# Kernel optimization log

Measured on AMD Instinct MI355X. Metric: run time of the kernel, lower is better.

The kernel has to match this reference:

```python
import jax, jax.numpy as jnp
import numpy as np


def gelu(x):
    # custom GELU classes in such repos typically implement the tanh approximation
    return jax.nn.gelu(x, approximate=True)


def setup_inputs() -> dict:
    key = jax.random.key(0)
    ks = jax.random.split(key, 16)
    B, N1, N2, D, H = 4, 1024, 1024, 256, 4
    prev = jax.random.normal(ks[0], (B, N1, D), dtype=jnp.float32)
    curr = jax.random.normal(ks[1], (B, N2, D), dtype=jnp.float32)
    edges = jax.random.randint(ks[2], (B, N1, N2), 0, 2).astype(jnp.int32)

    def lin(k, fan_in, fan_out):
        kw, kb = jax.random.split(k)
        s = 1.0 / np.sqrt(fan_in)
        W = jax.random.uniform(kw, (fan_in, fan_out), jnp.float32, -s, s)
        b = jax.random.uniform(kb, (fan_out,), jnp.float32, -s, s)
        return W, b

    W_pre, b_pre = lin(ks[3], D, 6)
    W_cur, b_cur = lin(ks[4], D, 6)
    W_fuse, b_fuse = lin(ks[5], 12, 4)
    W_ffn, b_ffn = lin(ks[6], 12, 8)
    W_fcc, b_fcc = lin(ks[7], 8, H)
    W_fcg, b_fcg = lin(ks[8], 8, D)
    return {"prev": prev, "curr": curr, "edges": edges,
            "W_pre": W_pre, "b_pre": b_pre, "W_cur": W_cur, "b_cur": b_cur,
            "W_fuse": W_fuse, "b_fuse": b_fuse, "W_ffn": W_ffn, "b_ffn": b_ffn,
            "W_fcc": W_fcc, "b_fcc": b_fcc, "W_fcg": W_fcg, "b_fcg": b_fcg}


def reference(prev, curr, edges, W_pre, b_pre, W_cur, b_cur,
              W_fuse, b_fuse, W_ffn, b_ffn, W_fcc, b_fcc, W_fcg, b_fcg):
    B, N1, D = prev.shape
    N2 = curr.shape[1]
    H = W_fcc.shape[1]
    Dh = D // H
    mask = edges != 0                                   # [B,N1,N2]

    bt_pre = prev @ W_pre + b_pre                       # [B,N1,6]
    bt_cur = curr @ W_cur + b_cur                       # [B,N2,6]
    pair = jnp.concatenate([
        jnp.broadcast_to(bt_pre[:, :, None, :], (B, N1, N2, 6)),
        jnp.broadcast_to(bt_cur[:, None, :, :], (B, N1, N2, 6))], axis=-1)
    c = gelu(pair) @ W_fuse + b_fuse                    # [B,N1,N2,4]
    c = jnp.where(mask[..., None], c, 0.0)

    e1 = (jnp.sum(edges, axis=1) + 1).astype(c.dtype)   # [B,N2]
    d = jnp.sum(c, axis=1)[:, None] / e1[:, None, :, None]
    d = jnp.broadcast_to(d, c.shape)
    e = jnp.broadcast_to(jnp.max(c, axis=1)[:, None], c.shape)
    fused = gelu(jnp.concatenate([c, d, e], axis=-1)) @ W_ffn + b_ffn  # [B,N1,N2,8]

    att = gelu(fused) @ W_fcc + b_fcc                   # [B,N1,N2,H]
    att = jnp.transpose(att, (0, 2, 1, 3))              # [B,N2,N1,H]
    maskT = jnp.transpose(mask, (0, 2, 1))              # [B,N2,N1]
    logits = jnp.where(maskT[..., None], att, -9e15)
    p = jax.nn.softmax(logits, axis=2)                  # softmax over N1 per head
    p = jnp.where(maskT[..., None], p, 0.0)
    # per-head aggregation: head i uses prev columns [i*Dh, (i+1)*Dh)
    res = jnp.einsum('bmnh,bnhd->bmhd', p, prev.reshape(B, N1, H, Dh)).reshape(B, N2, D)

    fused_m = jnp.where(mask[..., None], fused, 0.0)
    g = jnp.sum(fused_m, axis=1) / e1[..., None]        # [B,N2,8]
    return res + gelu(g) @ W_fcg + b_fcg                # [B,N2,D]
```

## Files before the change

### kernel.cpp

```cpp
#include <hip/hip_runtime.h>


using bf16x8 = __attribute__((ext_vector_type(8))) short;
using f32x4  = __attribute__((ext_vector_type(4))) float;
typedef float v2f __attribute__((ext_vector_type(2)));

__device__ __forceinline__ v2f pk_fma(v2f a, v2f b, v2f c){
    return __builtin_elementwise_fma(a, b, c);
}

__device__ __forceinline__ float gelu_f(float x){
    float x2 = x*x;
    float tt = x * __builtin_fmaf(0.044715f, x2, 1.0f);
    float e  = exp2f(-2.3022082f * tt);
    return x * __builtin_amdgcn_rcpf(1.0f + e);
}

__device__ __forceinline__ v2f gelu2(v2f x){
    v2f x2 = x*x;
    v2f tt = x * pk_fma((v2f){0.044715f,0.044715f}, x2, (v2f){1.0f,1.0f});
    float e0 = exp2f(-2.3022082f * tt[0]);
    float e1 = exp2f(-2.3022082f * tt[1]);
    v2f r = { __builtin_amdgcn_rcpf(1.0f + e0),
              __builtin_amdgcn_rcpf(1.0f + e1) };
    return x * r;
}

__device__ __forceinline__ unsigned short f2bf(float f){
    unsigned int u = __float_as_uint(f);
    u += 0x7FFFu + ((u >> 16) & 1u);
    return (unsigned short)(u >> 16);
}

__global__ __launch_bounds__(256) void k_rowsT(
    const float* __restrict__ prev, const float* __restrict__ curr,
    const float* __restrict__ W_pre, const float* __restrict__ b_pre,
    const float* __restrict__ W_cur, const float* __restrict__ b_cur,
    const float* __restrict__ W_fuse, const float* __restrict__ b_fuse,
    float* __restrict__ u_ws, float* __restrict__ v_ws,
    unsigned short* __restrict__ prevT)
{
    __shared__ float tile[64][65];
    int t = threadIdx.x;
    if (blockIdx.x < 2048){
        int gid  = blockIdx.x * 256 + t;
        int wave = gid >> 6;
        int lane = t & 63;
        bool isPrev = wave < 4096;
        int row = isPrev ? wave : (wave - 4096);
        const float* xrow = (isPrev ? prev : curr) + (size_t)row * 256;
        const float* W  = isPrev ? W_pre : W_cur;
        const float* bv = isPrev ? b_pre : b_cur;

        float4 x4 = *reinterpret_cast<const float4*>(xrow + lane*4);
        const float* Wl = W + lane*24;
        float p[6];
        #pragma unroll
        for (int k=0;k<6;++k)
            p[k] = x4.x*Wl[k] + x4.y*Wl[6+k] + x4.z*Wl[12+k] + x4.w*Wl[18+k];
        #pragma unroll
        for (int off=32; off>=1; off>>=1){
            #pragma unroll
            for (int k=0;k<6;++k) p[k] += __shfl_xor(p[k], off, 64);
        }
        if (lane == 0){
            float g[6];
            #pragma unroll
            for(int k=0;k<6;++k) g[k] = gelu_f(p[k] + bv[k]);
            int rb = isPrev ? 0 : 6;
            float o[4];
            #pragma unroll
            for(int kk=0;kk<4;++kk){
                float a = isPrev ? 0.0f : b_fuse[kk];
                #pragma unroll
                for(int k=0;k<6;++k) a += g[k]*W_fuse[(rb+k)*4+kk];
                o[kk]=a;
            }
            float* dst = (isPrev ? u_ws : v_ws) + (size_t)row*4;
            *reinterpret_cast<float4*>(dst) = make_float4(o[0],o[1],o[2],o[3]);
        }
    } else {
        int pbid = blockIdx.x - 2048;
        int b  = pbid >> 6;
        int it = (pbid >> 2) & 15;
        int dt = pbid & 3;
        int i0 = it*64, d0 = dt*64;
        int col = t & 63, rw = t >> 6;
        #pragma unroll
        for (int r = 0; r < 16; ++r){
            int row = rw + 4*r;
            tile[row][col] = prev[((size_t)b*1024 + i0 + row)*256 + d0 + col];
        }
        __syncthreads();
        #pragma unroll
        for (int r = 0; r < 16; ++r){
            int drow = rw + 4*r;
            prevT[((size_t)b*256 + d0 + drow)*1024 + i0 + col]
                = f2bf(tile[col][drow]);
        }
    }
}

__global__ __launch_bounds__(256) void k_cols(
    const int* __restrict__ edges,
    const float* __restrict__ u_ws, const float* __restrict__ v_ws,
    const float* __restrict__ W_ffn, const float* __restrict__ b_ffn,
    float* __restrict__ Gd_ws, float* __restrict__ cnt_ws)
{
    int b  = blockIdx.x >> 6;
    int j0 = (blockIdx.x & 63) * 16;
    int t  = threadIdx.x;
    int jq = t & 3, sl = t >> 2;
    const int*   eb = edges + (size_t)b*1048576 + j0 + jq*4;
    const float* ub = u_ws + (size_t)b*4096;

    int   cnt[4] = {0,0,0,0};
    float S[4][4] = {{0.f}};
    float M[4][4];
    #pragma unroll
    for (int q=0;q<4;++q)
        #pragma unroll
        for (int k=0;k<4;++k) M[q][k] = -3.4e38f;

    #pragma unroll 4
    for (int ii=0; ii<16; ++ii){
        int i = sl*16 + ii;
        int4   e4 = *reinterpret_cast<const int4*>(eb + (size_t)i*1024);
        float4 u4 = *reinterpret_cast<const float4*>(ub + i*4);
        float uu[4] = {u4.x,u4.y,u4.z,u4.w};
        int   ee[4] = {e4.x,e4.y,e4.z,e4.w};
        #pragma unroll
        for (int q=0;q<4;++q){
            bool mk = ee[q]!=0;
            cnt[q] += mk ? 1 : 0;
            #pragma unroll
            for (int k=0;k<4;++k){
                S[q][k] += mk ? uu[k] : 0.0f;
                M[q][k]  = mk ? fmaxf(M[q][k],uu[k]) : M[q][k];
            }
        }
    }
    __shared__ float rS[64][16][4];
    __shared__ float rM[64][16][4];
    __shared__ int   rC[64][16];
    #pragma unroll
    for (int q=0;q<4;++q){
        int c = jq*4+q;
        #pragma unroll
        for (int k=0;k<4;++k){ rS[sl][c][k]=S[q][k]; rM[sl][c][k]=M[q][k]; }
        rC[sl][c]=cnt[q];
    }
    __syncthreads();
    float aS[4], aM[4]; int aC=0; int c2=0, hf=0;
    if (t < 128){
        c2 = t & 15; hf = t >> 4;
        #pragma unroll
        for(int k=0;k<4;++k){ aS[k]=0.f; aM[k]=-3.4e38f; }
        for (int s2=hf*8; s2<hf*8+8; ++s2){
            aC += rC[s2][c2];
            #pragma unroll
            for(int k=0;k<4;++k){ aS[k]+=rS[s2][c2][k]; aM[k]=fmaxf(aM[k],rM[s2][c2][k]); }
        }
    }
    __syncthreads();
    if (t < 128){
        rC[hf][c2]=aC;
        #pragma unroll
        for(int k=0;k<4;++k){ rS[hf][c2][k]=aS[k]; rM[hf][c2][k]=aM[k]; }
    }
    __syncthreads();
    if (t < 16){
        int cc=0; float Sa[4]={0,0,0,0};
        float Ma[4]={-3.4e38f,-3.4e38f,-3.4e38f,-3.4e38f};
        for (int s2=0;s2<8;++s2){
            cc += rC[s2][t];
            #pragma unroll
            for(int k=0;k<4;++k){ Sa[k]+=rS[s2][t][k]; Ma[k]=fmaxf(Ma[k],rM[s2][t][k]); }
        }
        size_t cj = (size_t)b*1024 + j0 + t;
        float4 v4 = *reinterpret_cast<const float4*>(v_ws + cj*4);
        float vv[4]={v4.x,v4.y,v4.z,v4.w};
        float cf = (float)cc, e1 = cf + 1.0f;
        float gd[4], ge[4];
        #pragma unroll
        for(int k=0;k<4;++k){
            float dk = (Sa[k] + cf*vv[k]) / e1;
            float ek;
            if (cc == 0) ek = 0.0f;
            else { float m1 = Ma[k]+vv[k]; ek = (cc < 1024) ? fmaxf(m1, 0.0f) : m1; }
            gd[k]=gelu_f(dk); ge[k]=gelu_f(ek);
        }
        #pragma unroll
        for(int kk=0;kk<8;++kk){
            float a = b_ffn[kk];
            #pragma unroll
            for(int k=0;k<4;++k)
                a += gd[k]*W_ffn[(4+k)*8+kk] + ge[k]*W_ffn[(8+k)*8+kk];
            Gd_ws[cj*8+kk]=a;
        }
        cnt_ws[cj]=cf;
    }
}

template<int SPLIT>
__global__ __launch_bounds__(256) void k_main(
    const unsigned short* __restrict__ prevT, const int* __restrict__ edges,
    const float* __restrict__ u_ws, const float* __restrict__ v_ws,
    const float* __restrict__ Gd_ws,
    const float* __restrict__ W_ffn, const float* __restrict__ W_fcc,
    const float* __restrict__ b_fcc,
    float* __restrict__ Pws, float* __restrict__ Sws, float* __restrict__ Tws)
{
    const int RPB = 1024/SPLIT;
    int bid = blockIdx.x;
    int sp  = bid & (SPLIT-1);
    int jt  = (bid / SPLIT) & 127;
    int b   = bid / (SPLIT*128);
    int j0  = jt*8;
    int t   = threadIdx.x;
    int lane = t & 63;
    int wv   = t >> 6;
    int jl_w = t & 7, il_w = t >> 3;

    __shared__ unsigned short wA[2][4096];
    __shared__ __align__(16) float sU[2][64][4];
    __shared__ float sV[8][4];
    __shared__ float sGd[8][8];

    if (t < 32) (&sV[0][0])[t]  = v_ws[((size_t)b*1024 + j0)*4 + t];
    if (t < 64) (&sGd[0][0])[t] = Gd_ws[((size_t)b*1024 + j0)*8 + t];
    {
        unsigned int* wz = (unsigned int*)wA;
        #pragma unroll
        for (int z=0; z<16; ++z) wz[t + z*256] = 0u;
    }

    const float LOG2E = 1.4426950408889634f;
    v2f W4p[4][4], Wfcp[8][2], bfcp[2];
    #pragma unroll
    for(int k=0;k<4;++k)
        #pragma unroll
        for(int q=0;q<4;++q)
            W4p[k][q] = (v2f){W_ffn[k*8+2*q], W_ffn[k*8+2*q+1]};
    #pragma unroll
    for(int kk=0;kk<8;++kk)
        #pragma unroll
        for(int p2=0;p2<2;++p2)
            Wfcp[kk][p2] = (v2f){W_fcc[kk*4+2*p2]*LOG2E, W_fcc[kk*4+2*p2+1]*LOG2E};
    #pragma unroll
    for(int p2=0;p2<2;++p2)
        bfcp[p2] = (v2f){b_fcc[2*p2]*LOG2E, b_fcc[2*p2+1]*LOG2E};

    f32x4 accm[4];
    #pragma unroll
    for (int tile=0;tile<4;++tile) accm[tile] = (f32x4){0.f,0.f,0.f,0.f};
    f32x4 accs = (f32x4){0.f,0.f,0.f,0.f};
    bf16x8 onesB;
    #pragma unroll
    for (int e=0;e<8;++e) onesB[e] = (short)0x3F80;
    v2f Tp01 = {0,0}, Tp23 = {0,0};

    const int* ebase = edges + (size_t)b*1048576 + j0;
    const int NCH = RPB/64;
    const int base_i0 = sp*RPB;

    int arow = lane & 15, kgrp = lane >> 4;
    int aoff0 = (((wv*16 + arow)*64 + kgrp*8)*2) ^ ((arow & 7) << 4);
    int aoff1 = aoff0 ^ 64;
    const unsigned short* pTbase = prevT
        + ((size_t)b*256 + wv*64 + arow)*1024 + base_i0 + kgrp*8;

    float su_r = u_ws[((size_t)b*1024 + base_i0)*4 + t];
    (&sU[0][0][0])[t] = su_r;
    int egr0 = ebase[(size_t)(base_i0+il_w   )*1024 + jl_w];
    int egr1 = ebase[(size_t)(base_i0+il_w+32)*1024 + jl_w];
    {
        int i0n = base_i0 + ((1 < NCH) ? 64 : 0);
        su_r = u_ws[((size_t)b*1024 + i0n)*4 + t];
    }
    __syncthreads();

    float4 v4p = *reinterpret_cast<const float4*>(&sV[jl_w][0]);
    float4 gd0 = *reinterpret_cast<const float4*>(&sGd[jl_w][0]);
    float4 gd1 = *reinterpret_cast<const float4*>(&sGd[jl_w][4]);

    for (int cc=0; cc<NCH; ++cc){
        int p = cc & 1;
        char* wAp = reinterpret_cast<char*>(wA) + p*8192;

        int eg_c[2] = {egr0, egr1};
        {
            int i0n = base_i0 + ((cc+1 < NCH) ? (cc+1)*64 : 0);
            egr0 = ebase[(size_t)(i0n+il_w   )*1024 + jl_w];
            egr1 = ebase[(size_t)(i0n+il_w+32)*1024 + jl_w];
        }

        #pragma unroll
        for (int r=0;r<2;++r){
            int il = il_w + 32*r;
            int eg = eg_c[r];
            float4 u4 = *reinterpret_cast<const float4*>(&sU[p][il][0]);
            v2f g01 = gelu2((v2f){u4.x + v4p.x, u4.y + v4p.y});
            v2f g23 = gelu2((v2f){u4.z + v4p.z, u4.w + v4p.w});
            float m = eg ? 1.0f : 0.0f;
            v2f mm = {m, m};
            Tp01 = pk_fma(mm, g01, Tp01);
            Tp23 = pk_fma(mm, g23, Tp23);
            v2f a0 = {gd0.x, gd0.y}, a1 = {gd0.z, gd0.w};
            v2f a2 = {gd1.x, gd1.y}, a3 = {gd1.z, gd1.w};
            v2f G0 = {g01[0], g01[0]}, G1 = {g01[1], g01[1]};
            v2f G2 = {g23[0], g23[0]}, G3 = {g23[1], g23[1]};
            a0 = pk_fma(G0, W4p[0][0], a0); a1 = pk_fma(G0, W4p[0][1], a1);
            a2 = pk_fma(G0, W4p[0][2], a2); a3 = pk_fma(G0, W4p[0][3], a3);
            a0 = pk_fma(G1, W4p[1][0], a0); a1 = pk_fma(G1, W4p[1][1], a1);
            a2 = pk_fma(G1, W4p[1][2], a2); a3 = pk_fma(G1, W4p[1][3], a3);
            a0 = pk_fma(G2, W4p[2][0], a0); a1 = pk_fma(G2, W4p[2][1], a1);
            a2 = pk_fma(G2, W4p[2][2], a2); a3 = pk_fma(G2, W4p[2][3], a3);
            a0 = pk_fma(G3, W4p[3][0], a0); a1 = pk_fma(G3, W4p[3][1], a1);
            a2 = pk_fma(G3, W4p[3][2], a2); a3 = pk_fma(G3, W4p[3][3], a3);
            v2f f01 = gelu2(a0), f23 = gelu2(a1);
            v2f f45 = gelu2(a2), f67 = gelu2(a3);
            v2f L01 = bfcp[0], L23 = bfcp[1];
            float fv[8] = {f01[0],f01[1],f23[0],f23[1],f45[0],f45[1],f67[0],f67[1]};
            #pragma unroll
            for (int kk=0;kk<8;++kk){
                v2f F = {fv[kk], fv[kk]};
                L01 = pk_fma(F, Wfcp[kk][0], L01);
                L23 = pk_fma(F, Wfcp[kk][1], L23);
            }
            float lg[4] = {L01[0], L01[1], L23[0], L23[1]};
            int low = ((jl_w*64 + il)*2) ^ (jl_w << 4);
            #pragma unroll
            for (int hh=0;hh<4;++hh){
                float wf = eg ? exp2f(lg[hh]) : 0.0f;
                *reinterpret_cast<unsigned short*>(wAp + hh*2048 + low) = f2bf(wf);
            }
        }

        (&sU[p^1][0][0])[t] = su_r;
        {
            int i0n2 = base_i0 + ((cc+2 < NCH) ? (cc+2)*64 : 0);
            su_r = u_ws[((size_t)b*1024 + i0n2)*4 + t];
        }
        __syncthreads();

        bf16x8 afr0 = *reinterpret_cast<const bf16x8*>(wAp + aoff0);
        bf16x8 afr1 = *reinterpret_cast<const bf16x8*>(wAp + aoff1);
        const unsigned short* pT = pTbase + (size_t)cc*64;
        #pragma unroll
        for (int tile=0; tile<4; ++tile){
            const unsigned short* pB = pT + (size_t)tile*16*1024;
            bf16x8 bfr0 = *reinterpret_cast<const bf16x8*>(pB);
            bf16x8 bfr1 = *reinterpret_cast<const bf16x8*>(pB + 32);
            accm[tile] = __builtin_amdgcn_mfma_f32_16x16x32_bf16(
                afr0, bfr0, accm[tile], 0, 0, 0);
            accm[tile] = __builtin_amdgcn_mfma_f32_16x16x32_bf16(
                afr1, bfr1, accm[tile], 0, 0, 0);
        }
        accs = __builtin_amdgcn_mfma_f32_16x16x32_bf16(afr0, onesB, accs, 0,0,0);
        accs = __builtin_amdgcn_mfma_f32_16x16x32_bf16(afr1, onesB, accs, 0,0,0);
    }

    size_t bp = ((size_t)b*128 + jt)*SPLIT + sp;

    float* sT4 = reinterpret_cast<float*>(wA);
    {
        float* ts = sT4 + (size_t)t*4;
        ts[0]=Tp01[0]; ts[1]=Tp01[1]; ts[2]=Tp23[0]; ts[3]=Tp23[1];
    }
    __syncthreads();
    if (t < 8){
        float T0=0,T1=0,T2=0,T3=0;
        for (int s2=0;s2<32;++s2){
            const float* p = sT4 + (size_t)(s2*8 + t)*4;
            T0+=p[0]; T1+=p[1]; T2+=p[2]; T3+=p[3];
        }
        float* td = Tws + (bp*8 + t)*4;
        td[0]=T0; td[1]=T1; td[2]=T2; td[3]=T3;
    }

    if (arow == 0 && kgrp < 2){
        #pragma unroll
        for (int r2=0; r2<4; ++r2)
            Sws[bp*32 + wv*8 + kgrp*4 + r2] = accs[r2];
    }
    if (kgrp < 2){
        #pragma unroll
        for (int tile=0; tile<4; ++tile){
            #pragma unroll
            for (int r2=0; r2<4; ++r2){
                int j   = kgrp*4 + r2;
                int dim = wv*64 + tile*16 + arow;
                Pws[((size_t)bp*8 + j)*256 + dim] = accm[tile][r2];
            }
        }
    }
}

template<int SPLIT>
__global__ __launch_bounds__(256) void k_merge(
    const float* __restrict__ Pws, const float* __restrict__ Sws,
    const float* __restrict__ Tws,
    const float* __restrict__ Gd_ws, const float* __restrict__ cnt_ws,
    const float* __restrict__ W_ffn, const float* __restrict__ W_fcg,
    const float* __restrict__ b_fcg, float* __restrict__ out)
{
    int b  = blockIdx.x >> 7;
    int jt = blockIdx.x & 127;
    int j0 = jt*8;
    int t  = threadIdx.x;
    int jl = t >> 5, hd = t & 31, h = hd >> 3, dq = hd & 7;
    __shared__ float sG[8][8];

    size_t bp0 = ((size_t)b*128 + jt)*SPLIT;
    float s = 0.0f, acc[8] = {0,0,0,0,0,0,0,0};
    #pragma unroll
    for (int sp2=0; sp2<SPLIT; ++sp2){
        const float* p = Pws + ((bp0+sp2)*8 + jl)*256 + hd*8;
        float4 p0 = *reinterpret_cast<const float4*>(p);
        float4 p1 = *reinterpret_cast<const float4*>(p+4);
        acc[0]+=p0.x; acc[1]+=p0.y; acc[2]+=p0.z; acc[3]+=p0.w;
        acc[4]+=p1.x; acc[5]+=p1.y; acc[6]+=p1.z; acc[7]+=p1.w;
        s += Sws[(bp0+sp2)*32 + h*8 + jl];
    }
    if (t < 8){
        float T[4] = {0,0,0,0};
        #pragma unroll
        for (int sp2=0; sp2<SPLIT; ++sp2){
            const float* tp = Tws + ((bp0+sp2)*8 + t)*4;
            #pragma unroll
            for (int k=0;k<4;++k) T[k]+=tp[k];
        }
        size_t cj = (size_t)b*1024 + j0 + t;
        float cf = cnt_ws[cj];
        float inv = __fdividef(1.0f, cf + 1.0f);
        #pragma unroll
        for (int kk=0;kk<8;++kk){
            float a = cf*Gd_ws[cj*8+kk];
            #pragma unroll
            for (int k=0;k<4;++k) a += T[k]*W_ffn[k*8+kk];
            sG[t][kk] = gelu_f(a*inv);
        }
    }
    __syncthreads();

    float rs = (s > 0.0f) ? (1.0f/s) : 0.0f;
    int col0 = h*64 + dq*8;
    float gg[8];
    #pragma unroll
    for (int kk=0;kk<8;++kk) gg[kk]=sG[jl][kk];
    float o[8];
    #pragma unroll
    for (int d2=0;d2<8;++d2){
        float a = b_fcg[col0+d2];
        #pragma unroll
        for (int kk=0;kk<8;++kk) a += gg[kk]*W_fcg[kk*256 + col0 + d2];
        o[d2] = acc[d2]*rs + a;
    }
    float* ob = out + ((size_t)b*1024 + j0 + jl)*256 + col0;
    float4* o4 = reinterpret_cast<float4*>(ob);
    o4[0] = make_float4(o[0],o[1],o[2],o[3]);
    o4[1] = make_float4(o[4],o[5],o[6],o[7]);
}

extern "C" void kernel_launch(void* const* d_in, const int* in_sizes, int n_in,
                              void* d_out, int out_size, void* d_ws, size_t ws_size,
                              hipStream_t stream)
{
    const float* prev  = (const float*)d_in[0];
    const float* curr  = (const float*)d_in[1];
    const int*   edges = (const int*)  d_in[2];
    const float* W_pre = (const float*)d_in[3];
    const float* b_pre = (const float*)d_in[4];
    const float* W_cur = (const float*)d_in[5];
    const float* b_cur = (const float*)d_in[6];
    const float* W_fuse= (const float*)d_in[7];
    const float* b_fuse= (const float*)d_in[8];
    const float* W_ffn = (const float*)d_in[9];
    const float* b_ffn = (const float*)d_in[10];
    const float* W_fcc = (const float*)d_in[11];
    const float* b_fcc = (const float*)d_in[12];
    const float* W_fcg = (const float*)d_in[13];
    const float* b_fcg = (const float*)d_in[14];
    float* out = (float*)d_out;

    float* u_ws   = (float*)d_ws;
    float* v_ws   = u_ws  + 16384;
    float* Gd_ws  = v_ws  + 16384;
    float* cnt_ws = Gd_ws + 32768;
    float* Pws    = cnt_ws + 4096;
    const size_t base_f = 16384 + 16384 + 32768 + 4096;

    const size_t p4  = (size_t)4*128*4*8*256;
    const size_t s4v = (size_t)4*128*4*32;
    const size_t t4  = (size_t)4*128*4*8*4;
    const size_t pT_f = (size_t)4*256*1024/2;
    const size_t need4 = (base_f + p4 + s4v + t4 + pT_f) * 4;
    const size_t p2 = p4/2, s2v = s4v/2, t2 = t4/2;
    const size_t need2 = (base_f + p2 + s2v + t2 + pT_f) * 4;
    const size_t p1 = p4/4, s1 = s4v/4, t1 = t4/4;

    if (ws_size >= need4){
        float* Sws = Pws + p4;
        float* Tws = Sws + s4v;
        unsigned short* prevT = (unsigned short*)(Tws + t4);
        k_rowsT<<<dim3(2304), dim3(256), 0, stream>>>(prev, curr, W_pre, b_pre,
            W_cur, b_cur, W_fuse, b_fuse, u_ws, v_ws, prevT);
        k_cols<<<dim3(256), dim3(256), 0, stream>>>(edges, u_ws, v_ws,
            W_ffn, b_ffn, Gd_ws, cnt_ws);
        k_main<4><<<dim3(2048), dim3(256), 0, stream>>>(prevT, edges, u_ws,
            v_ws, Gd_ws, W_ffn, W_fcc, b_fcc, Pws, Sws, Tws);
        k_merge<4><<<dim3(512), dim3(256), 0, stream>>>(Pws, Sws, Tws, Gd_ws,
            cnt_ws, W_ffn, W_fcg, b_fcg, out);
    } else if (ws_size >= need2){
        float* Sws = Pws + p2;
        float* Tws = Sws + s2v;
        unsigned short* prevT = (unsigned short*)(Tws + t2);
        k_rowsT<<<dim3(2304), dim3(256), 0, stream>>>(prev, curr, W_pre, b_pre,
            W_cur, b_cur, W_fuse, b_fuse, u_ws, v_ws, prevT);
        k_cols<<<dim3(256), dim3(256), 0, stream>>>(edges, u_ws, v_ws,
            W_ffn, b_ffn, Gd_ws, cnt_ws);
        k_main<2><<<dim3(1024), dim3(256), 0, stream>>>(prevT, edges, u_ws,
            v_ws, Gd_ws, W_ffn, W_fcc, b_fcc, Pws, Sws, Tws);
        k_merge<2><<<dim3(512), dim3(256), 0, stream>>>(Pws, Sws, Tws, Gd_ws,
            cnt_ws, W_ffn, W_fcg, b_fcg, out);
    } else {
        float* Sws = Pws + p1;
        float* Tws = Sws + s1;
        unsigned short* prevT = (unsigned short*)(Tws + t1);
        k_rowsT<<<dim3(2304), dim3(256), 0, stream>>>(prev, curr, W_pre, b_pre,
            W_cur, b_cur, W_fuse, b_fuse, u_ws, v_ws, prevT);
        k_cols<<<dim3(256), dim3(256), 0, stream>>>(edges, u_ws, v_ws,
            W_ffn, b_ffn, Gd_ws, cnt_ws);
        k_main<1><<<dim3(512), dim3(256), 0, stream>>>(prevT, edges, u_ws,
            v_ws, Gd_ws, W_ffn, W_fcc, b_fcc, Pws, Sws, Tws);
        k_merge<1><<<dim3(512), dim3(256), 0, stream>>>(Pws, Sws, Tws, Gd_ws,
            cnt_ws, W_ffn, W_fcg, b_fcg, out);
    }
}
```

Before: 74.36 us.

## Widen k_main column tile from 8 to 16 to fill MFMA rows

Each k_main block now handles 16 target columns instead of 8, so the 16-row MFMA A fragment is fully used rather than half zero-padded, and the grid is halved. Each thread computes four edge rows per chunk instead of two, and the zero-init of the shared weight tile is dropped because all 16 rows are now written. The prevT B-fragment loads are amortized over twice as many columns. The merge kernel indexing and workspace sizes are adapted to the new layout. The cost is more per-thread work, more registers and fewer blocks to spread across CUs.

```diff
diff --git a/kernel.cpp b/kernel.cpp
--- a/kernel.cpp
+++ b/kernel.cpp
@@ -214,26 +214,21 @@
     const int RPB = 1024/SPLIT;
     int bid = blockIdx.x;
     int sp  = bid & (SPLIT-1);
-    int jt  = (bid / SPLIT) & 127;
-    int b   = bid / (SPLIT*128);
-    int j0  = jt*8;
+    int jt  = (bid / SPLIT) & 63;
+    int b   = bid / (SPLIT*64);
+    int j0  = jt*16;
     int t   = threadIdx.x;
     int lane = t & 63;
     int wv   = t >> 6;
-    int jl_w = t & 7, il_w = t >> 3;
+    int jl_w = t & 15, il_w = t >> 4;
 
     __shared__ unsigned short wA[2][4096];
     __shared__ __align__(16) float sU[2][64][4];
-    __shared__ float sV[8][4];
-    __shared__ float sGd[8][8];
-
-    if (t < 32) (&sV[0][0])[t]  = v_ws[((size_t)b*1024 + j0)*4 + t];
-    if (t < 64) (&sGd[0][0])[t] = Gd_ws[((size_t)b*1024 + j0)*8 + t];
-    {
-        unsigned int* wz = (unsigned int*)wA;
-        #pragma unroll
-        for (int z=0; z<16; ++z) wz[t + z*256] = 0u;
-    }
+    __shared__ float sV[16][4];
+    __shared__ float sGd[16][8];
+
+    if (t < 64)  (&sV[0][0])[t]  = v_ws[((size_t)b*1024 + j0)*4 + t];
+    if (t < 128) (&sGd[0][0])[t] = Gd_ws[((size_t)b*1024 + j0)*8 + t];
 
     const float LOG2E = 1.4426950408889634f;
     v2f W4p[4][4], Wfcp[8][2], bfcp[2];
@@ -272,8 +267,10 @@
 
     float su_r = u_ws[((size_t)b*1024 + base_i0)*4 + t];
     (&sU[0][0][0])[t] = su_r;
-    int egr0 = ebase[(size_t)(base_i0+il_w   )*1024 + jl_w];
-    int egr1 = ebase[(size_t)(base_i0+il_w+32)*1024 + jl_w];
+    int egr[4];
+    #pragma unroll
+    for (int r=0;r<4;++r)
+        egr[r] = ebase[(size_t)(base_i0 + il_w + 16*r)*1024 + jl_w];
     {
         int i0n = base_i0 + ((1 < NCH) ? 64 : 0);
         su_r = u_ws[((size_t)b*1024 + i0n)*4 + t];
@@ -288,16 +285,17 @@
         int p = cc & 1;
         char* wAp = reinterpret_cast<char*>(wA) + p*8192;
 
-        int eg_c[2] = {egr0, egr1};
+        int eg_c[4] = {egr[0], egr[1], egr[2], egr[3]};
         {
             int i0n = base_i0 + ((cc+1 < NCH) ? (cc+1)*64 : 0);
-            egr0 = ebase[(size_t)(i0n+il_w   )*1024 + jl_w];
-            egr1 = ebase[(size_t)(i0n+il_w+32)*1024 + jl_w];
-        }
-
-        #pragma unroll
-        for (int r=0;r<2;++r){
-            int il = il_w + 32*r;
+            #pragma unroll
+            for (int r=0;r<4;++r)
+                egr[r] = ebase[(size_t)(i0n + il_w + 16*r)*1024 + jl_w];
+        }
+
+        #pragma unroll
+        for (int r=0;r<4;++r){
+            int il = il_w + 16*r;
             int eg = eg_c[r];
             float4 u4 = *reinterpret_cast<const float4*>(&sU[p][il][0]);
             v2f g01 = gelu2((v2f){u4.x + v4p.x, u4.y + v4p.y});
@@ -329,7 +327,7 @@
                 L23 = pk_fma(F, Wfcp[kk][1], L23);
             }
             float lg[4] = {L01[0], L01[1], L23[0], L23[1]};
-            int low = ((jl_w*64 + il)*2) ^ (jl_w << 4);
+            int low = ((jl_w*64 + il)*2) ^ ((jl_w & 7) << 4);
             #pragma unroll
             for (int hh=0;hh<4;++hh){
                 float wf = eg ? exp2f(lg[hh]) : 0.0f;
@@ -361,7 +359,7 @@
         accs = __builtin_amdgcn_mfma_f32_16x16x32_bf16(afr1, onesB, accs, 0,0,0);
     }
 
-    size_t bp = ((size_t)b*128 + jt)*SPLIT + sp;
+    size_t bp = ((size_t)b*64 + jt)*SPLIT + sp;
 
     float* sT4 = reinterpret_cast<float*>(wA);
     {
@@ -369,29 +367,29 @@
         ts[0]=Tp01[0]; ts[1]=Tp01[1]; ts[2]=Tp23[0]; ts[3]=Tp23[1];
     }
     __syncthreads();
-    if (t < 8){
+    if (t < 16){
         float T0=0,T1=0,T2=0,T3=0;
-        for (int s2=0;s2<32;++s2){
-            const float* p = sT4 + (size_t)(s2*8 + t)*4;
+        for (int s2=0;s2<16;++s2){
+            const float* p = sT4 + (size_t)(s2*16 + t)*4;
             T0+=p[0]; T1+=p[1]; T2+=p[2]; T3+=p[3];
         }
-        float* td = Tws + (bp*8 + t)*4;
+        float* td = Tws + (bp*16 + t)*4;
         td[0]=T0; td[1]=T1; td[2]=T2; td[3]=T3;
     }
 
-    if (arow == 0 && kgrp < 2){
+    if (arow == 0){
         #pragma unroll
         for (int r2=0; r2<4; ++r2)
-            Sws[bp*32 + wv*8 + kgrp*4 + r2] = accs[r2];
-    }
-    if (kgrp < 2){
+            Sws[bp*64 + wv*16 + kgrp*4 + r2] = accs[r2];
+    }
+    {
         #pragma unroll
         for (int tile=0; tile<4; ++tile){
             #pragma unroll
             for (int r2=0; r2<4; ++r2){
                 int j   = kgrp*4 + r2;
                 int dim = wv*64 + tile*16 + arow;
-                Pws[((size_t)bp*8 + j)*256 + dim] = accm[tile][r2];
+                Pws[((size_t)bp*16 + j)*256 + dim] = accm[tile][r2];
             }
         }
     }
@@ -405,29 +403,32 @@
     const float* __restrict__ W_ffn, const float* __restrict__ W_fcg,
     const float* __restrict__ b_fcg, float* __restrict__ out)
 {
-    int b  = blockIdx.x >> 7;
-    int jt = blockIdx.x & 127;
-    int j0 = jt*8;
+    int b   = blockIdx.x >> 7;
+    int jt8 = blockIdx.x & 127;
+    int jt16 = jt8 >> 1;
+    int cb  = (jt8 & 1) * 8;
+    int j0  = jt8*8;
     int t  = threadIdx.x;
     int jl = t >> 5, hd = t & 31, h = hd >> 3, dq = hd & 7;
+    int col = cb + jl;
     __shared__ float sG[8][8];
 
-    size_t bp0 = ((size_t)b*128 + jt)*SPLIT;
+    size_t bp0 = ((size_t)b*64 + jt16)*SPLIT;
     float s = 0.0f, acc[8] = {0,0,0,0,0,0,0,0};
     #pragma unroll
     for (int sp2=0; sp2<SPLIT; ++sp2){
-        const float* p = Pws + ((bp0+sp2)*8 + jl)*256 + hd*8;
+        const float* p = Pws + ((bp0+sp2)*16 + col)*256 + hd*8;
         float4 p0 = *reinterpret_cast<const float4*>(p);
         float4 p1 = *reinterpret_cast<const float4*>(p+4);
         acc[0]+=p0.x; acc[1]+=p0.y; acc[2]+=p0.z; acc[3]+=p0.w;
         acc[4]+=p1.x; acc[5]+=p1.y; acc[6]+=p1.z; acc[7]+=p1.w;
-        s += Sws[(bp0+sp2)*32 + h*8 + jl];
+        s += Sws[(bp0+sp2)*64 + h*16 + col];
     }
     if (t < 8){
         float T[4] = {0,0,0,0};
         #pragma unroll
         for (int sp2=0; sp2<SPLIT; ++sp2){
-            const float* tp = Tws + ((bp0+sp2)*8 + t)*4;
+            const float* tp = Tws + ((bp0+sp2)*16 + cb + t)*4;
             #pragma unroll
             for (int k=0;k<4;++k) T[k]+=tp[k];
         }
@@ -491,9 +492,9 @@
     float* Pws    = cnt_ws + 4096;
     const size_t base_f = 16384 + 16384 + 32768 + 4096;
 
-    const size_t p4  = (size_t)4*128*4*8*256;
-    const size_t s4v = (size_t)4*128*4*32;
-    const size_t t4  = (size_t)4*128*4*8*4;
+    const size_t p4  = (size_t)1024*16*256;
+    const size_t s4v = (size_t)1024*64;
+    const size_t t4  = (size_t)1024*16*4;
     const size_t pT_f = (size_t)4*256*1024/2;
     const size_t need4 = (base_f + p4 + s4v + t4 + pT_f) * 4;
     const size_t p2 = p4/2, s2v = s4v/2, t2 = t4/2;
@@ -508,7 +509,7 @@
             W_cur, b_cur, W_fuse, b_fuse, u_ws, v_ws, prevT);
         k_cols<<<dim3(256), dim3(256), 0, stream>>>(edges, u_ws, v_ws,
             W_ffn, b_ffn, Gd_ws, cnt_ws);
-        k_main<4><<<dim3(2048), dim3(256), 0, stream>>>(prevT, edges, u_ws,
+        k_main<4><<<dim3(1024), dim3(256), 0, stream>>>(prevT, edges, u_ws,
             v_ws, Gd_ws, W_ffn, W_fcc, b_fcc, Pws, Sws, Tws);
         k_merge<4><<<dim3(512), dim3(256), 0, stream>>>(Pws, Sws, Tws, Gd_ws,
             cnt_ws, W_ffn, W_fcg, b_fcg, out);
@@ -520,7 +521,7 @@
             W_cur, b_cur, W_fuse, b_fuse, u_ws, v_ws, prevT);
         k_cols<<<dim3(256), dim3(256), 0, stream>>>(edges, u_ws, v_ws,
             W_ffn, b_ffn, Gd_ws, cnt_ws);
-        k_main<2><<<dim3(1024), dim3(256), 0, stream>>>(prevT, edges, u_ws,
+        k_main<2><<<dim3(512), dim3(256), 0, stream>>>(prevT, edges, u_ws,
             v_ws, Gd_ws, W_ffn, W_fcc, b_fcc, Pws, Sws, Tws);
         k_merge<2><<<dim3(512), dim3(256), 0, stream>>>(Pws, Sws, Tws, Gd_ws,
             cnt_ws, W_ffn, W_fcg, b_fcg, out);
@@ -532,7 +533,7 @@
             W_cur, b_cur, W_fuse, b_fuse, u_ws, v_ws, prevT);
         k_cols<<<dim3(256), dim3(256), 0, stream>>>(edges, u_ws, v_ws,
             W_ffn, b_ffn, Gd_ws, cnt_ws);
-        k_main<1><<<dim3(512), dim3(256), 0, stream>>>(prevT, edges, u_ws,
+        k_main<1><<<dim3(256), dim3(256), 0, stream>>>(prevT, edges, u_ws,
             v_ws, Gd_ws, W_ffn, W_fcc, b_fcc, Pws, Sws, Tws);
         k_merge<1><<<dim3(512), dim3(256), 0, stream>>>(Pws, Sws, Tws, Gd_ws,
             cnt_ws, W_ffn, W_fcg, b_fcg, out);
```

After: 69.61 us. -6.4%, faster.
